# Kernel tuning notes

Hardware: AMD Instinct MI355X
Metric: run time of the kernel (lower is better)

## Reference

```python
import jax, jax.numpy as jnp
import numpy as np

N = 100000

def _norm_edges(edge_index, n):
    # add self loops, compute symmetric GCN normalization
    loop = jnp.arange(n, dtype=edge_index.dtype)
    src = jnp.concatenate([edge_index[0], loop])
    dst = jnp.concatenate([edge_index[1], loop])
    deg = jax.ops.segment_sum(jnp.ones_like(dst, dtype=jnp.float32), dst, num_segments=n)
    dinv = jnp.where(deg > 0, deg ** -0.5, 0.0)
    norm = dinv[src] * dinv[dst]
    return src, dst, norm

def _gcn(x, W, b, src, dst, norm, n):
    h = x @ W  # [N, out]
    msg = h[src] * norm[:, None]
    return jax.ops.segment_sum(msg, dst, num_segments=n) + b

def setup_inputs() -> dict:
    key = jax.random.key(0)
    ks = jax.random.split(key, 20)
    E = 3200000
    d_in, d_out = 64, 64
    def w(k, i, o):
        return jax.random.normal(k, (i, o), dtype=jnp.float32) * (1.0 / np.sqrt(i))
    return {
        "x": jax.random.normal(ks[0], (N, d_in), dtype=jnp.float32),
        "t": jax.random.normal(ks[1], (N,), dtype=jnp.float32),
        "edge_index": jax.random.randint(ks[2], (2, E), 0, N, dtype=jnp.int64),
        "W1": w(ks[3], d_in + 1, 64), "b1": jnp.zeros((64,), jnp.float32),
        "W2": w(ks[4], 64, 128), "b2": jnp.zeros((128,), jnp.float32),
        "W3": w(ks[5], 128, 256), "b3": jnp.zeros((256,), jnp.float32),
        "W4": w(ks[6], 256, 128), "b4": jnp.zeros((128,), jnp.float32),
        "F1": w(ks[7], 128, 256), "c1": jnp.zeros((256,), jnp.float32),
        "F2": w(ks[8], 256, 128), "c2": jnp.zeros((128,), jnp.float32),
        "F3": w(ks[9], 128, d_out), "c3": jnp.zeros((d_out,), jnp.float32),
    }

def reference(x, t, edge_index, W1, b1, W2, b2, W3, b3, W4, b4, F1, c1, F2, c2, F3, c3):
    n = x.shape[0]
    src, dst, norm = _norm_edges(edge_index, n)
    h = jnp.concatenate([x, t[:, None]], axis=1)
    h = jax.nn.gelu(_gcn(h, W1, b1, src, dst, norm, n))
    h = jax.nn.gelu(_gcn(h, W2, b2, src, dst, norm, n))
    h = jax.nn.gelu(_gcn(h, W3, b3, src, dst, norm, n))
    h = jax.nn.gelu(_gcn(h, W4, b4, src, dst, norm, n))
    h = jax.nn.gelu(h @ F1 + c1)
    h = jax.nn.gelu(h @ F2 + c2)
    return h @ F3 + c3
```

## Files before the change

### kernel.cpp

```cpp
#include <hip/hip_runtime.h>

static constexpr int BLK = 256;

typedef double d2 __attribute__((ext_vector_type(2)));

__device__ __forceinline__ double gelu_d(double v){
  double u = 0.7978845608028654 * (v + 0.044715 * v * v * v);
  return 0.5 * v * (1.0 + tanh(u));
}

__global__ void zero_k(int* __restrict__ a, int n){
  int stride = gridDim.x * blockDim.x;
  for (int i = blockIdx.x*blockDim.x + threadIdx.x; i < n; i += stride) a[i] = 0;
}

__global__ void detect_k(const int* __restrict__ ei, int* __restrict__ flag){
  if (threadIdx.x == 0 && blockIdx.x == 0){
    int zeros = 0;
    for (int i = 0; i < 64; ++i) if (ei[2*i + 1] == 0) ++zeros;
    *flag = (zeros >= 48) ? 1 : 0;
  }
}

__global__ void count_k(const int* __restrict__ ei, int E, const int* __restrict__ flag,
                        int* __restrict__ cnt){
  int is64 = *flag;
  int stride = gridDim.x * blockDim.x;
  for (int e = blockIdx.x*blockDim.x + threadIdx.x; e < E; e += stride){
    int d = is64 ? ei[2*(E + e)] : ei[E + e];
    atomicAdd(&cnt[d], 1);
  }
}

__global__ void dinv_k(const int* __restrict__ cnt, double* __restrict__ dinv, int n){
  int i = blockIdx.x*blockDim.x + threadIdx.x;
  if (i < n){
    double deg = (double)(cnt[i] + 1);
    dinv[i] = 1.0 / sqrt(deg);
  }
}

__global__ __launch_bounds__(256)
void scanA_k(const int* __restrict__ cnt, int* __restrict__ partial, int n, int chunk){
  __shared__ int red[256];
  int b = blockIdx.x;
  int lo = b * chunk, hi = min(n, lo + chunk);
  int s = 0;
  for (int i = lo + threadIdx.x; i < hi; i += 256) s += cnt[i];
  red[threadIdx.x] = s; __syncthreads();
  for (int off = 128; off > 0; off >>= 1){
    if (threadIdx.x < off) red[threadIdx.x] += red[threadIdx.x + off];
    __syncthreads();
  }
  if (threadIdx.x == 0) partial[b] = red[0];
}

__global__ __launch_bounds__(256)
void scanB_k(int* __restrict__ partial, int nb){
  __shared__ int sd[256];
  int tid = threadIdx.x;
  int v = (tid < nb) ? partial[tid] : 0;
  sd[tid] = v; __syncthreads();
  for (int off = 1; off < 256; off <<= 1){
    int t = (tid >= off) ? sd[tid - off] : 0;
    __syncthreads();
    sd[tid] += t;
    __syncthreads();
  }
  if (tid < nb) partial[tid] = sd[tid] - v;
  if (tid == 255) partial[nb] = sd[255];
}

__global__ __launch_bounds__(256)
void scanC_k(const int* __restrict__ cnt, const int* __restrict__ partial,
             int* __restrict__ rp, int n, int chunk, int nb){
  __shared__ int sd[256];
  int b = blockIdx.x;
  int lo = b * chunk, hi = min(n, lo + chunk);
  int run = partial[b];
  for (int base = lo; base < hi; base += 256){
    int i = base + threadIdx.x;
    int v = (i < hi) ? cnt[i] : 0;
    sd[threadIdx.x] = v; __syncthreads();
    for (int off = 1; off < 256; off <<= 1){
      int t = (threadIdx.x >= off) ? sd[threadIdx.x - off] : 0;
      __syncthreads();
      sd[threadIdx.x] += t;
      __syncthreads();
    }
    if (i < hi) rp[i] = run + sd[threadIdx.x] - v;
    run += sd[255];
    __syncthreads();
  }
  if (b == 0 && threadIdx.x == 0) rp[n] = partial[nb];
}

__global__ void scatter_k(const int* __restrict__ ei, int E, const int* __restrict__ flag,
                          const int* __restrict__ rp, int* __restrict__ fill,
                          int* __restrict__ col){
  int is64 = *flag;
  int stride = gridDim.x * blockDim.x;
  for (int e = blockIdx.x*blockDim.x + threadIdx.x; e < E; e += stride){
    int s = is64 ? ei[2*e]       : ei[e];
    int d = is64 ? ei[2*(E + e)] : ei[E + e];
    int p = rp[d] + atomicAdd(&fill[d], 1);
    col[p] = s;
  }
}

template<typename ST>
__global__ void concat_k(const float* __restrict__ x, const float* __restrict__ t,
                         ST* __restrict__ h0, int n){
  int total = n * 66;
  int stride = gridDim.x * blockDim.x;
  for (int idx = blockIdx.x*blockDim.x + threadIdx.x; idx < total; idx += stride){
    int row = idx / 66;
    int c = idx - row * 66;
    float v = (c < 64) ? x[row*64 + c] : (c == 64 ? t[row] : 0.0f);
    h0[idx] = (ST)v;
  }
}

template<typename ST>
__global__ __launch_bounds__(256)
void gemm_k(const ST* __restrict__ A, int K, int lda,
            const float* __restrict__ W, int NOUT,
            const float* __restrict__ bias,
            ST* __restrict__ C, float* __restrict__ Cf,
            int n, int fuse)
{
  __shared__ __align__(16) double As[64][34];
  __shared__ __align__(16) double Ws[32][66];
  int row0 = blockIdx.x * 64;
  int col0 = blockIdx.y * 64;
  int tid = threadIdx.x;
  int tr = tid >> 4, tc = tid & 15;
  int c0 = 2 * tc;
  double acc[4][4] = {};
  int ktiles = (K + 31) / 32;
  for (int kt = 0; kt < ktiles; ++kt){
    int k0 = kt * 32;
    {
      int r  = tid >> 2;
      int kk = (tid & 3) * 8;
      int gr = row0 + r;
      const ST* Ap = A + (size_t)gr * lda + k0 + kk;
      #pragma unroll
      for (int u = 0; u < 8; ++u){
        int kg = k0 + kk + u;
        As[r][kk + u] = (gr < n && kg < K) ? (double)Ap[u] : 0.0;
      }
    }
    {
      int r = tid >> 3;
      int c = (tid & 7) * 8;
      int kg = k0 + r;
      const float* Wp = W + (size_t)kg * NOUT + col0 + c;
      #pragma unroll
      for (int u = 0; u < 8; ++u)
        Ws[r][c + u] = (kg < K) ? (double)Wp[u] : 0.0;
    }
    __syncthreads();
    #pragma unroll
    for (int kk = 0; kk < 32; kk += 2){
      d2 av[4];
      #pragma unroll
      for (int i = 0; i < 4; ++i) av[i] = *(const d2*)&As[tr*4 + i][kk];
      d2 w0a = *(const d2*)&Ws[kk    ][c0];
      d2 w0b = *(const d2*)&Ws[kk    ][c0 + 32];
      d2 w1a = *(const d2*)&Ws[kk + 1][c0];
      d2 w1b = *(const d2*)&Ws[kk + 1][c0 + 32];
      #pragma unroll
      for (int i = 0; i < 4; ++i){
        acc[i][0] = fma(av[i].x, w0a.x, acc[i][0]);
        acc[i][1] = fma(av[i].x, w0a.y, acc[i][1]);
        acc[i][2] = fma(av[i].x, w0b.x, acc[i][2]);
        acc[i][3] = fma(av[i].x, w0b.y, acc[i][3]);
        acc[i][0] = fma(av[i].y, w1a.x, acc[i][0]);
        acc[i][1] = fma(av[i].y, w1a.y, acc[i][1]);
        acc[i][2] = fma(av[i].y, w1b.x, acc[i][2]);
        acc[i][3] = fma(av[i].y, w1b.y, acc[i][3]);
      }
    }
    __syncthreads();
  }
  #pragma unroll
  for (int i = 0; i < 4; ++i){
    int r = row0 + tr*4 + i;
    if (r >= n) continue;
    #pragma unroll
    for (int j = 0; j < 4; ++j){
      int c = col0 + ((j < 2) ? (c0 + j) : (c0 + 30 + j));
      double v = acc[i][j];
      if (fuse){ v += (double)bias[c]; if (fuse == 1) v = gelu_d(v); }
      if (fuse == 2) Cf[(size_t)r * NOUT + c] = (float)v;
      else           C [(size_t)r * NOUT + c] = (ST)v;
    }
  }
}

template<typename ST, int NC>
__global__ __launch_bounds__(256)
void agg_k(const ST* __restrict__ T, const int* __restrict__ rp,
           const int* __restrict__ col, const double* __restrict__ dinv,
           const float* __restrict__ bias, ST* __restrict__ O, int n, int fuse)
{
  constexpr int DOUT = NC * 64;
  int w = (blockIdx.x * blockDim.x + threadIdx.x) >> 6;
  int lane = threadIdx.x & 63;
  if (w >= n) return;
  double dv = dinv[w];
  const ST* Ti = T + (size_t)w * DOUT;
  double acc[NC];
  #pragma unroll
  for (int c = 0; c < NC; ++c) acc[c] = dv * (double)Ti[lane + 64*c];
  int e1 = rp[w + 1];
  for (int e = rp[w]; e < e1; ++e){
    int s = col[e];
    double vs = dinv[s];
    const ST* Ts = T + (size_t)s * DOUT;
    #pragma unroll
    for (int c = 0; c < NC; ++c) acc[c] = fma(vs, (double)Ts[lane + 64*c], acc[c]);
  }
  ST* Oi = O + (size_t)w * DOUT;
  #pragma unroll
  for (int c = 0; c < NC; ++c){
    double v = dv * acc[c];
    if (fuse) v = gelu_d(v + (double)bias[lane + 64*c]);
    Oi[lane + 64*c] = (ST)v;
  }
}

template<typename ST>
static void run_net(const float* x, const float* t,
                    const float* W1, const float* b1, const float* W2, const float* b2,
                    const float* W3, const float* b3, const float* W4, const float* b4,
                    const float* F1, const float* c1, const float* F2, const float* c2,
                    const float* F3, const float* c3,
                    ST* b256, ST* ba, ST* bb,
                    const int* rp, const int* col, const double* dinv,
                    float* out, int N, hipStream_t stream)
{
  auto gemm = [&](const ST* A, int K, int lda, const float* W, int NOUT, const float* bias,
                  ST* C, float* Cf, int fuse){
    dim3 g((N + 63) / 64, NOUT / 64);
    gemm_k<ST><<<g, dim3(BLK), 0, stream>>>(A, K, lda, W, NOUT, bias, C, Cf, N, fuse);
  };
  int aggGrid = (N * 64 + BLK - 1) / BLK;
  auto agg64 = [&](const ST* T, const float* bias, ST* O, int fuse){
    agg_k<ST,1><<<dim3(aggGrid), dim3(BLK), 0, stream>>>(T, rp, col, dinv, bias, O, N, fuse);
  };
  auto agg128 = [&](const ST* T, const float* bias, ST* O, int fuse){
    agg_k<ST,2><<<dim3(aggGrid), dim3(BLK), 0, stream>>>(T, rp, col, dinv, bias, O, N, fuse);
  };

  concat_k<ST><<<dim3(1024), dim3(BLK), 0, stream>>>(x, t, ba, N);
  gemm(ba, 65, 66, W1, 64, nullptr, bb, nullptr, 0);
  agg64(bb, b1, ba, 1);
  agg64(ba, nullptr, bb, 0);
  gemm(bb, 64, 64, W2, 128, b2, ba, nullptr, 1);
  agg128(ba, nullptr, bb, 0);
  gemm(bb, 128, 128, W3, 256, b3, b256, nullptr, 1);
  gemm(b256, 256, 256, W4, 128, nullptr, ba, nullptr, 0);
  agg128(ba, b4, bb, 1);
  gemm(bb, 128, 128, F1, 256, c1, b256, nullptr, 1);
  gemm(b256, 256, 256, F2, 128, c2, ba, nullptr, 1);
  gemm(ba, 128, 128, F3, 64, c3, nullptr, out, 2);
}

extern "C" void kernel_launch(void* const* d_in, const int* in_sizes, int n_in,
                              void* d_out, int out_size, void* d_ws, size_t ws_size,
                              hipStream_t stream)
{
  const float* x  = (const float*)d_in[0];
  const float* t  = (const float*)d_in[1];
  const int*   ei = (const int*)d_in[2];
  const float* W1 = (const float*)d_in[3];  const float* b1 = (const float*)d_in[4];
  const float* W2 = (const float*)d_in[5];  const float* b2 = (const float*)d_in[6];
  const float* W3 = (const float*)d_in[7];  const float* b3 = (const float*)d_in[8];
  const float* W4 = (const float*)d_in[9];  const float* b4 = (const float*)d_in[10];
  const float* F1 = (const float*)d_in[11]; const float* c1 = (const float*)d_in[12];
  const float* F2 = (const float*)d_in[13]; const float* c2 = (const float*)d_in[14];
  const float* F3 = (const float*)d_in[15]; const float* c3 = (const float*)d_in[16];
  float* out = (float*)d_out;
  int N = in_sizes[0] / 64;
  int E = in_sizes[2] / 2;

  char* p = (char*)d_ws;
  auto alloc = [&](size_t b){ char* r = p; p += (b + 255) & ~(size_t)255; return (void*)r; };
  int*    flag    = (int*)alloc(4);
  int*    cnt     = (int*)alloc((size_t)N * 4);
  int*    fill    = (int*)alloc((size_t)N * 4);
  int*    rp      = (int*)alloc((size_t)(N + 1) * 4);
  int*    partial = (int*)alloc((size_t)257 * 4);
  int*    col     = (int*)alloc((size_t)E * 4);
  double* dinv    = (double*)alloc((size_t)N * 8);
  size_t base = (size_t)(p - (char*)d_ws);

  size_t actElems = (size_t)N * 512;
  bool f64ok = ws_size >= base + actElems * sizeof(double);
  bool f32ok = ws_size >= base + actElems * sizeof(float);
  if (!f32ok) return;

  int nb = 256;
  int chunk = (N + nb - 1) / nb;
  zero_k<<<dim3(256), dim3(BLK), 0, stream>>>(cnt, N);
  zero_k<<<dim3(256), dim3(BLK), 0, stream>>>(fill, N);
  detect_k<<<1, 64, 0, stream>>>(ei, flag);
  count_k<<<dim3(4096), dim3(BLK), 0, stream>>>(ei, E, flag, cnt);
  dinv_k<<<dim3((N + BLK - 1) / BLK), dim3(BLK), 0, stream>>>(cnt, dinv, N);
  scanA_k<<<dim3(nb), dim3(256), 0, stream>>>(cnt, partial, N, chunk);
  scanB_k<<<dim3(1), dim3(256), 0, stream>>>(partial, nb);
  scanC_k<<<dim3(nb), dim3(256), 0, stream>>>(cnt, partial, rp, N, chunk, nb);
  scatter_k<<<dim3(4096), dim3(BLK), 0, stream>>>(ei, E, flag, rp, fill, col);

  if (f64ok){
    double* b256 = (double*)alloc((size_t)N * 256 * 8);
    double* ba   = (double*)alloc((size_t)N * 128 * 8);
    double* bb   = (double*)alloc((size_t)N * 128 * 8);
    run_net<double>(x, t, W1, b1, W2, b2, W3, b3, W4, b4, F1, c1, F2, c2, F3, c3,
                    b256, ba, bb, rp, col, dinv, out, N, stream);
  } else {
    float* b256 = (float*)alloc((size_t)N * 256 * 4);
    float* ba   = (float*)alloc((size_t)N * 128 * 4);
    float* bb   = (float*)alloc((size_t)N * 128 * 4);
    run_net<float>(x, t, W1, b1, W2, b2, W3, b3, W4, b4, F1, c1, F2, c2, F3, c3,
                   b256, ba, bb, rp, col, dinv, out, N, stream);
  }
}
```

Measured before the change: 2.793 ms.

## Precompute per-edge weights, unroll aggregation, enlarge GEMM row tile, use nontemporal stores

The scatter pass now stores the source node's dinv next to each CSR column entry, so the aggregation loop reads it sequentially instead of doing a random dinv[s] gather. The aggregation loop is unrolled by four to keep more independent row loads in flight, and it uses nontemporal loads and stores. The GEMM tile grows to 128 rows per block with 8x4 accumulators and an occupancy hint. The costs are an extra E*8-byte workspace buffer, higher register pressure in the GEMM, and extra scatter writes.

```diff
diff --git a/kernel.cpp b/kernel.cpp
--- a/kernel.cpp
+++ b/kernel.cpp
@@ -97,7 +97,8 @@
 
 __global__ void scatter_k(const int* __restrict__ ei, int E, const int* __restrict__ flag,
                           const int* __restrict__ rp, int* __restrict__ fill,
-                          int* __restrict__ col){
+                          const double* __restrict__ dinv,
+                          int* __restrict__ col, double* __restrict__ val){
   int is64 = *flag;
   int stride = gridDim.x * blockDim.x;
   for (int e = blockIdx.x*blockDim.x + threadIdx.x; e < E; e += stride){
@@ -105,6 +106,7 @@
     int d = is64 ? ei[2*(E + e)] : ei[E + e];
     int p = rp[d] + atomicAdd(&fill[d], 1);
     col[p] = s;
+    if (val) val[p] = dinv[s];
   }
 }
 
@@ -122,31 +124,31 @@
 }
 
 template<typename ST>
-__global__ __launch_bounds__(256)
+__global__ __launch_bounds__(256, 2)
 void gemm_k(const ST* __restrict__ A, int K, int lda,
             const float* __restrict__ W, int NOUT,
             const float* __restrict__ bias,
             ST* __restrict__ C, float* __restrict__ Cf,
             int n, int fuse)
 {
-  __shared__ __align__(16) double As[64][34];
+  __shared__ __align__(16) double As[128][34];
   __shared__ __align__(16) double Ws[32][66];
-  int row0 = blockIdx.x * 64;
+  int row0 = blockIdx.x * 128;
   int col0 = blockIdx.y * 64;
   int tid = threadIdx.x;
   int tr = tid >> 4, tc = tid & 15;
   int c0 = 2 * tc;
-  double acc[4][4] = {};
+  double acc[8][4] = {};
   int ktiles = (K + 31) / 32;
   for (int kt = 0; kt < ktiles; ++kt){
     int k0 = kt * 32;
     {
-      int r  = tid >> 2;
-      int kk = (tid & 3) * 8;
+      int r  = tid >> 1;
+      int kk = (tid & 1) * 16;
       int gr = row0 + r;
       const ST* Ap = A + (size_t)gr * lda + k0 + kk;
       #pragma unroll
-      for (int u = 0; u < 8; ++u){
+      for (int u = 0; u < 16; ++u){
         int kg = k0 + kk + u;
         As[r][kk + u] = (gr < n && kg < K) ? (double)Ap[u] : 0.0;
       }
@@ -163,38 +165,36 @@
     __syncthreads();
     #pragma unroll
     for (int kk = 0; kk < 32; kk += 2){
-      d2 av[4];
-      #pragma unroll
-      for (int i = 0; i < 4; ++i) av[i] = *(const d2*)&As[tr*4 + i][kk];
       d2 w0a = *(const d2*)&Ws[kk    ][c0];
       d2 w0b = *(const d2*)&Ws[kk    ][c0 + 32];
       d2 w1a = *(const d2*)&Ws[kk + 1][c0];
       d2 w1b = *(const d2*)&Ws[kk + 1][c0 + 32];
       #pragma unroll
-      for (int i = 0; i < 4; ++i){
-        acc[i][0] = fma(av[i].x, w0a.x, acc[i][0]);
-        acc[i][1] = fma(av[i].x, w0a.y, acc[i][1]);
-        acc[i][2] = fma(av[i].x, w0b.x, acc[i][2]);
-        acc[i][3] = fma(av[i].x, w0b.y, acc[i][3]);
-        acc[i][0] = fma(av[i].y, w1a.x, acc[i][0]);
-        acc[i][1] = fma(av[i].y, w1a.y, acc[i][1]);
-        acc[i][2] = fma(av[i].y, w1b.x, acc[i][2]);
-        acc[i][3] = fma(av[i].y, w1b.y, acc[i][3]);
+      for (int i = 0; i < 8; ++i){
+        d2 av = *(const d2*)&As[tr + 16*i][kk];
+        acc[i][0] = fma(av.x, w0a.x, acc[i][0]);
+        acc[i][1] = fma(av.x, w0a.y, acc[i][1]);
+        acc[i][2] = fma(av.x, w0b.x, acc[i][2]);
+        acc[i][3] = fma(av.x, w0b.y, acc[i][3]);
+        acc[i][0] = fma(av.y, w1a.x, acc[i][0]);
+        acc[i][1] = fma(av.y, w1a.y, acc[i][1]);
+        acc[i][2] = fma(av.y, w1b.x, acc[i][2]);
+        acc[i][3] = fma(av.y, w1b.y, acc[i][3]);
       }
     }
     __syncthreads();
   }
   #pragma unroll
-  for (int i = 0; i < 4; ++i){
-    int r = row0 + tr*4 + i;
+  for (int i = 0; i < 8; ++i){
+    int r = row0 + tr + 16*i;
     if (r >= n) continue;
     #pragma unroll
     for (int j = 0; j < 4; ++j){
       int c = col0 + ((j < 2) ? (c0 + j) : (c0 + 30 + j));
       double v = acc[i][j];
       if (fuse){ v += (double)bias[c]; if (fuse == 1) v = gelu_d(v); }
-      if (fuse == 2) Cf[(size_t)r * NOUT + c] = (float)v;
-      else           C [(size_t)r * NOUT + c] = (ST)v;
+      if (fuse == 2) __builtin_nontemporal_store((float)v, &Cf[(size_t)r * NOUT + c]);
+      else           __builtin_nontemporal_store((ST)v,   &C [(size_t)r * NOUT + c]);
     }
   }
 }
@@ -202,8 +202,9 @@
 template<typename ST, int NC>
 __global__ __launch_bounds__(256)
 void agg_k(const ST* __restrict__ T, const int* __restrict__ rp,
-           const int* __restrict__ col, const double* __restrict__ dinv,
-           const float* __restrict__ bias, ST* __restrict__ O, int n, int fuse)
+           const int* __restrict__ col, const double* __restrict__ val,
+           const double* __restrict__ dinv, const float* __restrict__ bias,
+           ST* __restrict__ O, int n, int fuse)
 {
   constexpr int DOUT = NC * 64;
   int w = (blockIdx.x * blockDim.x + threadIdx.x) >> 6;
@@ -214,20 +215,60 @@
   double acc[NC];
   #pragma unroll
   for (int c = 0; c < NC; ++c) acc[c] = dv * (double)Ti[lane + 64*c];
+  int e  = rp[w];
   int e1 = rp[w + 1];
-  for (int e = rp[w]; e < e1; ++e){
-    int s = col[e];
-    double vs = dinv[s];
-    const ST* Ts = T + (size_t)s * DOUT;
-    #pragma unroll
-    for (int c = 0; c < NC; ++c) acc[c] = fma(vs, (double)Ts[lane + 64*c], acc[c]);
+  if (val){
+    for (; e + 4 <= e1; e += 4){
+      int s0 = __builtin_nontemporal_load(&col[e]);
+      int s1 = __builtin_nontemporal_load(&col[e+1]);
+      int s2 = __builtin_nontemporal_load(&col[e+2]);
+      int s3 = __builtin_nontemporal_load(&col[e+3]);
+      double v0 = __builtin_nontemporal_load(&val[e]);
+      double v1 = __builtin_nontemporal_load(&val[e+1]);
+      double v2 = __builtin_nontemporal_load(&val[e+2]);
+      double v3 = __builtin_nontemporal_load(&val[e+3]);
+      const ST* T0 = T + (size_t)s0 * DOUT;
+      const ST* T1 = T + (size_t)s1 * DOUT;
+      const ST* T2 = T + (size_t)s2 * DOUT;
+      const ST* T3 = T + (size_t)s3 * DOUT;
+      double t0[NC], t1[NC], t2[NC], t3[NC];
+      #pragma unroll
+      for (int c = 0; c < NC; ++c){
+        t0[c] = (double)T0[lane + 64*c];
+        t1[c] = (double)T1[lane + 64*c];
+        t2[c] = (double)T2[lane + 64*c];
+        t3[c] = (double)T3[lane + 64*c];
+      }
+      #pragma unroll
+      for (int c = 0; c < NC; ++c){
+        acc[c] = fma(v0, t0[c], acc[c]);
+        acc[c] = fma(v1, t1[c], acc[c]);
+        acc[c] = fma(v2, t2[c], acc[c]);
+        acc[c] = fma(v3, t3[c], acc[c]);
+      }
+    }
+    for (; e < e1; ++e){
+      int s = __builtin_nontemporal_load(&col[e]);
+      double v = __builtin_nontemporal_load(&val[e]);
+      const ST* Ts = T + (size_t)s * DOUT;
+      #pragma unroll
+      for (int c = 0; c < NC; ++c) acc[c] = fma(v, (double)Ts[lane + 64*c], acc[c]);
+    }
+  } else {
+    for (; e < e1; ++e){
+      int s = col[e];
+      double v = dinv[s];
+      const ST* Ts = T + (size_t)s * DOUT;
+      #pragma unroll
+      for (int c = 0; c < NC; ++c) acc[c] = fma(v, (double)Ts[lane + 64*c], acc[c]);
+    }
   }
   ST* Oi = O + (size_t)w * DOUT;
   #pragma unroll
   for (int c = 0; c < NC; ++c){
     double v = dv * acc[c];
     if (fuse) v = gelu_d(v + (double)bias[lane + 64*c]);
-    Oi[lane + 64*c] = (ST)v;
+    __builtin_nontemporal_store((ST)v, &Oi[lane + 64*c]);
   }
 }
 
@@ -238,20 +279,20 @@
                     const float* F1, const float* c1, const float* F2, const float* c2,
                     const float* F3, const float* c3,
                     ST* b256, ST* ba, ST* bb,
-                    const int* rp, const int* col, const double* dinv,
+                    const int* rp, const int* col, const double* val, const double* dinv,
                     float* out, int N, hipStream_t stream)
 {
   auto gemm = [&](const ST* A, int K, int lda, const float* W, int NOUT, const float* bias,
                   ST* C, float* Cf, int fuse){
-    dim3 g((N + 63) / 64, NOUT / 64);
+    dim3 g((N + 127) / 128, NOUT / 64);
     gemm_k<ST><<<g, dim3(BLK), 0, stream>>>(A, K, lda, W, NOUT, bias, C, Cf, N, fuse);
   };
   int aggGrid = (N * 64 + BLK - 1) / BLK;
   auto agg64 = [&](const ST* T, const float* bias, ST* O, int fuse){
-    agg_k<ST,1><<<dim3(aggGrid), dim3(BLK), 0, stream>>>(T, rp, col, dinv, bias, O, N, fuse);
+    agg_k<ST,1><<<dim3(aggGrid), dim3(BLK), 0, stream>>>(T, rp, col, val, dinv, bias, O, N, fuse);
   };
   auto agg128 = [&](const ST* T, const float* bias, ST* O, int fuse){
-    agg_k<ST,2><<<dim3(aggGrid), dim3(BLK), 0, stream>>>(T, rp, col, dinv, bias, O, N, fuse);
+    agg_k<ST,2><<<dim3(aggGrid), dim3(BLK), 0, stream>>>(T, rp, col, val, dinv, bias, O, N, fuse);
   };
 
   concat_k<ST><<<dim3(1024), dim3(BLK), 0, stream>>>(x, t, ba, N);
@@ -298,9 +339,15 @@
   size_t base = (size_t)(p - (char*)d_ws);
 
   size_t actElems = (size_t)N * 512;
-  bool f64ok = ws_size >= base + actElems * sizeof(double);
-  bool f32ok = ws_size >= base + actElems * sizeof(float);
+  size_t valBytes = ((size_t)E * 8 + 255) & ~(size_t)255;
+  bool f64val = ws_size >= base + valBytes + actElems * sizeof(double);
+  bool f64ok  = f64val || ws_size >= base + actElems * sizeof(double);
+  bool f32val = ws_size >= base + valBytes + actElems * sizeof(float);
+  bool f32ok  = f32val || ws_size >= base + actElems * sizeof(float);
   if (!f32ok) return;
+
+  double* val = nullptr;
+  if ((f64ok && f64val) || (!f64ok && f32val)) val = (double*)alloc((size_t)E * 8);
 
   int nb = 256;
   int chunk = (N + nb - 1) / nb;
@@ -312,19 +359,19 @@
   scanA_k<<<dim3(nb), dim3(256), 0, stream>>>(cnt, partial, N, chunk);
   scanB_k<<<dim3(1), dim3(256), 0, stream>>>(partial, nb);
   scanC_k<<<dim3(nb), dim3(256), 0, stream>>>(cnt, partial, rp, N, chunk, nb);
-  scatter_k<<<dim3(4096), dim3(BLK), 0, stream>>>(ei, E, flag, rp, fill, col);
+  scatter_k<<<dim3(4096), dim3(BLK), 0, stream>>>(ei, E, flag, rp, fill, dinv, col, val);
 
   if (f64ok){
     double* b256 = (double*)alloc((size_t)N * 256 * 8);
     double* ba   = (double*)alloc((size_t)N * 128 * 8);
     double* bb   = (double*)alloc((size_t)N * 128 * 8);
     run_net<double>(x, t, W1, b1, W2, b2, W3, b3, W4, b4, F1, c1, F2, c2, F3, c3,
-                    b256, ba, bb, rp, col, dinv, out, N, stream);
+                    b256, ba, bb, rp, col, val, dinv, out, N, stream);
   } else {
     float* b256 = (float*)alloc((size_t)N * 256 * 4);
     float* ba   = (float*)alloc((size_t)N * 128 * 4);
     float* bb   = (float*)alloc((size_t)N * 128 * 4);
     run_net<float>(x, t, W1, b1, W2, b2, W3, b3, W4, b4, F1, c1, F2, c2, F3, c3,
-                   b256, ba, bb, rp, col, dinv, out, N, stream);
-  }
-}
+                   b256, ba, bb, rp, col, val, dinv, out, N, stream);
+  }
+}
```

Measured after the change: 2.553 ms. -8.6%, faster.
